# Performance work log

Hardware: AMD Instinct MI355X
Metric: run time of the kernel (lower is better)

## Reference

```python
import jax, jax.numpy as jnp
import numpy as np

N_NODES = 10000
N_EDGES = 80000
IN_DIM = 1024
HID = 4096
OUT = 256


def sage_conv(x, src, dst, W_l, b_l, W_r, num_nodes):
    # mean aggregation of source-node features onto target nodes
    msg = x[src]                                            # [E, D] gather
    agg = jax.ops.segment_sum(msg, dst, num_segments=num_nodes)   # [N, D]
    cnt = jax.ops.segment_sum(jnp.ones((src.shape[0],), x.dtype), dst,
                              num_segments=num_nodes)       # [N]
    mean = agg / jnp.clip(cnt, 1.0)[:, None]                # isolated nodes -> 0
    # lin_l(mean) + lin_r(x); lin_r has no bias in PyG SAGEConv
    return mean @ W_l.T + b_l + x @ W_r.T


def setup_inputs() -> dict:
    key = jax.random.key(0)
    ks = jax.random.split(key, 6)
    x = jax.random.normal(ks[0], (N_NODES, IN_DIM), dtype=jnp.float32)
    edge_index = jax.random.randint(ks[1], (2, N_EDGES), 0, N_NODES, dtype=jnp.int32)
    s1 = 1.0 / np.sqrt(IN_DIM)
    s2 = 1.0 / np.sqrt(HID)
    W1_l = jax.random.normal(ks[2], (HID, IN_DIM), dtype=jnp.float32) * s1
    b1_l = jnp.zeros((HID,), jnp.float32)
    W1_r = jax.random.normal(ks[3], (HID, IN_DIM), dtype=jnp.float32) * s1
    W2_l = jax.random.normal(ks[4], (OUT, HID), dtype=jnp.float32) * s2
    b2_l = jnp.zeros((OUT,), jnp.float32)
    W2_r = jax.random.normal(ks[5], (OUT, HID), dtype=jnp.float32) * s2
    return {"x": x, "edge_index": edge_index, "W1_l": W1_l, "b1_l": b1_l,
            "W1_r": W1_r, "W2_l": W2_l, "b2_l": b2_l, "W2_r": W2_r}


def reference(x, edge_index, W1_l, b1_l, W1_r, W2_l, b2_l, W2_r):
    src, dst = edge_index[0], edge_index[1]
    h = sage_conv(x, src, dst, W1_l, b1_l, W1_r, N_NODES)   # [N, 4096]
    h = jax.nn.relu(h)
    # dropout is identity in eval mode
    out = sage_conv(h, src, dst, W2_l, b2_l, W2_r, N_NODES)  # [N, 256]
    return jax.nn.log_softmax(out, axis=1)
```

## Files before the change

### kernel.cpp

```cpp
#include <hip/hip_runtime.h>
#include <cstdint>
#include <cstddef>

#define DEVINL __device__ __forceinline__

typedef __bf16 bf16x8 __attribute__((ext_vector_type(8)));
typedef float f32x4 __attribute__((ext_vector_type(4)));

static constexpr int NN = 10000;
static constexpr int NE = 80000;
static constexpr int IN_DIM = 1024;
static constexpr int HID = 4096;
static constexpr int OUTD = 256;
static constexpr int M_PAD = 10112;

DEVINL unsigned short f2bf(float f) {
  unsigned int u = __builtin_bit_cast(unsigned int, f);
  u += 0x7fffu + ((u >> 16) & 1u);
  return (unsigned short)(u >> 16);
}
DEVINL float bf2f(unsigned short h) {
  unsigned int u = ((unsigned int)h) << 16;
  return __builtin_bit_cast(float, u);
}

DEVINL void ld_lds16(const void* g, void* l) {
  __builtin_amdgcn_global_load_lds(
      (const __attribute__((address_space(1))) unsigned int*)g,
      (__attribute__((address_space(3))) unsigned int*)l, 16, 0, 0);
}

static constexpr int PREP_B1 = 8192;
static constexpr int PREP_B2 = PREP_B1 + 2048;
static constexpr int PREP_B3 = PREP_B2 + 10000;
static constexpr int PREP_NB = PREP_B3 + 313;

__global__ __launch_bounds__(256) void prep_kernel(
    const float* __restrict__ W1l, const float* __restrict__ W1r,
    const float* __restrict__ W2l, const float* __restrict__ W2r,
    const float* __restrict__ x, const int* __restrict__ dst,
    unsigned short* __restrict__ w1cat, unsigned short* __restrict__ w2cat,
    unsigned short* __restrict__ x_bf, int* __restrict__ deg) {
  int b = blockIdx.x;
  int t = threadIdx.x;
  if (b < PREP_B1) {
    int g = b * 256 + t;
    int n = g >> 9;
    int kg = g & 511;
    const float* s = (kg < 256) ? (W1l + (size_t)n * 1024 + kg * 4)
                                : (W1r + (size_t)n * 1024 + (kg - 256) * 4);
    float4 v = *(const float4*)s;
    ushort4 p = {f2bf(v.x), f2bf(v.y), f2bf(v.z), f2bf(v.w)};
    ((ushort4*)w1cat)[g] = p;
  } else if (b < PREP_B2) {
    int g = (b - PREP_B1) * 256 + t;
    int n = g >> 10;
    int kg = g & 1023;
    const float* s = (n < 256) ? (W2l + (size_t)n * 4096 + kg * 4)
                               : (W2r + (size_t)(n - 256) * 4096 + kg * 4);
    float4 v = *(const float4*)s;
    ushort4 p = {f2bf(v.x), f2bf(v.y), f2bf(v.z), f2bf(v.w)};
    ((ushort4*)w2cat)[g] = p;
  } else if (b < PREP_B3) {
    int g = (b - PREP_B2) * 256 + t;
    int i = g >> 8;
    int kg = g & 255;
    float4 v = ((const float4*)(x + (size_t)i * IN_DIM))[kg];
    ushort4 p = {f2bf(v.x), f2bf(v.y), f2bf(v.z), f2bf(v.w)};
    ((ushort4*)(x_bf + (size_t)i * IN_DIM))[kg] = p;
  } else {
    int e = (b - PREP_B3) * 256 + t;
    if (e < NE) atomicAdd(&deg[dst[e]], 1);
  }
}

__global__ __launch_bounds__(1024) void scan_kernel(const int* __restrict__ deg,
                                                    int* __restrict__ offs,
                                                    int* __restrict__ cur) {
  __shared__ int part[1024];
  constexpr int NPT = 10;
  int t = threadIdx.x;
  int base = t * NPT;
  int s = 0;
  for (int j = 0; j < NPT; ++j) {
    int n = base + j;
    s += (n < NN) ? deg[n] : 0;
  }
  part[t] = s;
  __syncthreads();
  for (int o = 1; o < 1024; o <<= 1) {
    int v = (t >= o) ? part[t - o] : 0;
    __syncthreads();
    part[t] += v;
    __syncthreads();
  }
  int pre = (t > 0) ? part[t - 1] : 0;
  for (int j = 0; j < NPT; ++j) {
    int n = base + j;
    if (n < NN) {
      offs[n] = pre;
      cur[n] = pre;
      pre += deg[n];
    }
  }
  if (t == 1023) offs[NN] = part[1023];
}

__global__ void bin_kernel(const int* __restrict__ src, const int* __restrict__ dst,
                           int* __restrict__ cur, int* __restrict__ csr) {
  int e = blockIdx.x * 256 + threadIdx.x;
  if (e < NE) {
    int p = atomicAdd(&cur[dst[e]], 1);
    csr[p] = src[e];
  }
}

__global__ __launch_bounds__(256) void gather1_kernel(unsigned short* __restrict__ x_bf,
                                                      const int* __restrict__ offs,
                                                      const int* __restrict__ csr,
                                                      unsigned short* __restrict__ A1) {
  int i = blockIdx.x;
  int t = threadIdx.x;
  unsigned short* row = A1 + (size_t)i * 1024;
  if (i >= NN) {
    ushort4 z = {0, 0, 0, 0};
    ((ushort4*)row)[t] = z;
    ((ushort4*)(x_bf + (size_t)i * 1024))[t] = z;
    return;
  }
  int beg = offs[i], end = offs[i + 1];
  float4 a0 = {0.f, 0.f, 0.f, 0.f}, a1 = {0.f, 0.f, 0.f, 0.f};
  int j = beg;
  for (; j + 2 <= end; j += 2) {
    int s0 = __builtin_amdgcn_readfirstlane(csr[j]);
    int s1 = __builtin_amdgcn_readfirstlane(csr[j + 1]);
    ushort4 u0 = ((const ushort4*)(x_bf + (size_t)s0 * IN_DIM))[t];
    ushort4 u1 = ((const ushort4*)(x_bf + (size_t)s1 * IN_DIM))[t];
    a0.x += bf2f(u0.x); a0.y += bf2f(u0.y); a0.z += bf2f(u0.z); a0.w += bf2f(u0.w);
    a1.x += bf2f(u1.x); a1.y += bf2f(u1.y); a1.z += bf2f(u1.z); a1.w += bf2f(u1.w);
  }
  if (j < end) {
    int s0 = __builtin_amdgcn_readfirstlane(csr[j]);
    ushort4 u0 = ((const ushort4*)(x_bf + (size_t)s0 * IN_DIM))[t];
    a0.x += bf2f(u0.x); a0.y += bf2f(u0.y); a0.z += bf2f(u0.z); a0.w += bf2f(u0.w);
  }
  float inv = 1.0f / (float)max(end - beg, 1);
  ushort4 pa = {f2bf((a0.x + a1.x) * inv), f2bf((a0.y + a1.y) * inv),
                f2bf((a0.z + a1.z) * inv), f2bf((a0.w + a1.w) * inv)};
  ((ushort4*)row)[t] = pa;
}

__global__ __launch_bounds__(256) void gemm1_pipe_kernel(
    const unsigned short* __restrict__ A,
    const unsigned short* __restrict__ A2,
    const unsigned short* __restrict__ Bt,
    const float* __restrict__ bias,
    unsigned short* __restrict__ C) {
  constexpr int BM = 128, BN = 128, BK = 64;
  constexpr int K = 2048, N = 4096;
  constexpr int NT = K / BK;
  constexpr int NUMM = 79, NUMN = 32, GM = 32, NPG = GM * NUMN;
  constexpr int TSZ = BM * BK;

  __shared__ unsigned short Asm[2 * TSZ];
  __shared__ unsigned short Bsm[3 * TSZ];

  const int pid = blockIdx.x;
  const int gid = pid / NPG;
  const int first_m = gid * GM;
  const int sz = (NUMM - first_m < GM) ? (NUMM - first_m) : GM;
  const int local = pid % NPG;
  const int pm = first_m + local % sz;
  const int pn = local / sz;
  const long tm0 = (long)pm * BM;
  const long tn0 = (long)pn * BN;

  const int tid = threadIdx.x;
  const int lane = tid & 63;
  const int wave = tid >> 6;
  const int quad = lane >> 4;
  const int l16 = lane & 15;
  const int l7 = l16 & 7;
  const int wm = (wave % 2) * 64;
  const int wn = (wave / 2) * 64;

  f32x4 acc[4][4];
#pragma unroll
  for (int i = 0; i < 4; ++i)
#pragma unroll
    for (int j = 0; j < 4; ++j) acc[i][j] = (f32x4){0.f, 0.f, 0.f, 0.f};

  size_t aOff[4], bOff[4];
#pragma unroll
  for (int s = 0; s < 4; ++s) {
    int c = s * 256 + tid;
    int r = c >> 3;
    int g = (c & 7) ^ (r & 7);
    aOff[s] = (size_t)(tm0 + r) * 1024 + g * 8;
    bOff[s] = (size_t)(tn0 + r) * K + g * 8;
  }

#define STAGE_A1(kt, ab)                                                            \
  {                                                                                 \
    const unsigned short* s_ = ((kt) < NT / 2) ? A : A2;                            \
    const int ka_ = ((kt) & (NT / 2 - 1)) * BK;                                     \
    _Pragma("unroll") for (int q_ = 0; q_ < 4; ++q_)                                \
        ld_lds16(s_ + aOff[q_] + ka_, Asm + (ab)*TSZ + q_ * 2048 + wave * 512);     \
  }
#define STAGE_B1(kt, bb)                                                            \
  {                                                                                 \
    const int k0_ = (kt)*BK;                                                        \
    _Pragma("unroll") for (int q_ = 0; q_ < 4; ++q_)                                \
        ld_lds16(Bt + bOff[q_] + k0_, Bsm + (bb)*TSZ + q_ * 2048 + wave * 512);     \
  }

  STAGE_A1(0, 0)
  STAGE_B1(0, 0)
  STAGE_B1(1, 1)

  int bb = 0;
  for (int t = 0; t < NT; ++t) {
    if (t + 1 < NT) STAGE_A1(t + 1, (t + 1) & 1)
    if (t + 2 < NT) {
      int bb2 = bb + 2;
      if (bb2 >= 3) bb2 -= 3;
      STAGE_B1(t + 2, bb2)
    }
    if (t + 2 < NT) {
      asm volatile("s_waitcnt vmcnt(12)" ::: "memory");
    } else if (t + 1 < NT) {
      asm volatile("s_waitcnt vmcnt(8)" ::: "memory");
    } else {
      asm volatile("s_waitcnt vmcnt(0)" ::: "memory");
    }
    __builtin_amdgcn_s_barrier();
    __builtin_amdgcn_sched_barrier(0);

    const unsigned short* As = Asm + (t & 1) * TSZ;
    const unsigned short* Bs = Bsm + bb * TSZ;
#pragma unroll
    for (int kk = 0; kk < 2; ++kk) {
      const int p = (kk * 4 + quad) ^ l7;
      bf16x8 af[4], bv[4];
#pragma unroll
      for (int i = 0; i < 4; ++i) af[i] = *(const bf16x8*)(As + (wm + i * 16 + l16) * BK + p * 8);
#pragma unroll
      for (int j = 0; j < 4; ++j) bv[j] = *(const bf16x8*)(Bs + (wn + j * 16 + l16) * BK + p * 8);
#pragma unroll
      for (int i = 0; i < 4; ++i)
#pragma unroll
        for (int j = 0; j < 4; ++j)
          acc[i][j] = __builtin_amdgcn_mfma_f32_16x16x32_bf16(af[i], bv[j], acc[i][j], 0, 0, 0);
    }
    __builtin_amdgcn_s_barrier();
    __builtin_amdgcn_sched_barrier(0);
    bb = (bb == 2) ? 0 : bb + 1;
  }
#undef STAGE_A1
#undef STAGE_B1

#pragma unroll
  for (int i = 0; i < 4; ++i) {
    long m0 = tm0 + wm + i * 16 + quad * 4;
#pragma unroll
    for (int j = 0; j < 4; ++j) {
      int n = (int)tn0 + wn + j * 16 + l16;
      float bvs = bias[n];
#pragma unroll
      for (int r = 0; r < 4; ++r) {
        float v = fmaxf(acc[i][j][r] + bvs, 0.0f);
        C[(size_t)(m0 + r) * N + n] = f2bf(v);
      }
    }
  }
}

template <int BM, int BN, int BK, int K, int KSPLIT, int N, int NUMM, int NUMN, int GM,
          int EPI, int NWY, bool ASPLIT>
__global__ __launch_bounds__(256) void gemm_kernel(const unsigned short* __restrict__ A,
                                                   const unsigned short* __restrict__ A2,
                                                   const unsigned short* __restrict__ Bt,
                                                   const float* __restrict__ bias,
                                                   void* __restrict__ C0out) {
  constexpr int MGR = 4 / NWY;
  constexpr int MI = BM / 16 / MGR;
  constexpr int NI = 4;
  constexpr int CPR = BK / 8;
  constexpr int SA = BM * CPR / 256;
  constexpr int SB = BN * CPR / 256;
  constexpr int KK = BK / 32;
  constexpr int KS = K / KSPLIT;
  constexpr int AS = ASPLIT ? K / 2 : K;
  __shared__ unsigned short Asm[BM * BK];
  __shared__ unsigned short Bsm[BN * BK];

  constexpr int NPG = GM * NUMN;
  const int pid = blockIdx.x;
  const int gid = pid / NPG;
  const int first_m = gid * GM;
  const int sz = (NUMM - first_m < GM) ? (NUMM - first_m) : GM;
  const int local = pid % NPG;
  const int pm = first_m + local % sz;
  const int pn = local / sz;
  const int koff = (KSPLIT > 1) ? (int)blockIdx.y * KS : 0;

  const int tid = threadIdx.x;
  const int lane = tid & 63;
  const int wave = tid >> 6;
  const int quad = lane >> 4;
  const int l16 = lane & 15;
  const int wm = (wave % MGR) * (BM / MGR);
  const int wn = (wave / MGR) * 64;
  const long tm0 = (long)pm * BM;
  const long tn0 = (long)pn * BN;

  f32x4 acc[MI][NI];
#pragma unroll
  for (int i = 0; i < MI; ++i)
#pragma unroll
    for (int j = 0; j < NI; ++j) acc[i][j] = (f32x4){0.f, 0.f, 0.f, 0.f};

  size_t aOff[SA];
  unsigned short* aDst[SA];
  const unsigned short* bSrc[SB];
  unsigned short* bDst[SB];
#pragma unroll
  for (int s = 0; s < SA; ++s) {
    int c = s * 256 + wave * 64 + lane;
    int r = c / CPR;
    int g = (c % CPR) ^ (r & 7);
    aOff[s] = (size_t)(tm0 + r) * AS + koff + g * 8;
    aDst[s] = Asm + s * 2048 + wave * 512;
  }
#pragma unroll
  for (int s = 0; s < SB; ++s) {
    int c = s * 256 + wave * 64 + lane;
    int r = c / CPR;
    int g = (c % CPR) ^ (r & 7);
    bSrc[s] = Bt + (size_t)(tn0 + r) * K + koff + g * 8;
    bDst[s] = Bsm + s * 2048 + wave * 512;
  }

  const int l7 = l16 & 7;

  for (int k0 = 0; k0 < KS; k0 += BK) {
    const unsigned short* ab = (!ASPLIT || k0 < K / 2) ? A : A2;
    const int ka = ASPLIT ? (k0 & (K / 2 - 1)) : k0;
#pragma unroll
    for (int s = 0; s < SA; ++s) ld_lds16(ab + aOff[s] + ka, aDst[s]);
#pragma unroll
    for (int s = 0; s < SB; ++s) ld_lds16(bSrc[s] + k0, bDst[s]);
    __syncthreads();

#pragma unroll
    for (int kk = 0; kk < KK; ++kk) {
      const int p = (kk * 4 + quad) ^ l7;
      bf16x8 af[MI], bv[NI];
#pragma unroll
      for (int i = 0; i < MI; ++i) {
        int ra = wm + i * 16 + l16;
        af[i] = *(const bf16x8*)(Asm + ra * BK + p * 8);
      }
#pragma unroll
      for (int j = 0; j < NI; ++j) {
        int rb = wn + j * 16 + l16;
        bv[j] = *(const bf16x8*)(Bsm + rb * BK + p * 8);
      }
#pragma unroll
      for (int i = 0; i < MI; ++i)
#pragma unroll
        for (int j = 0; j < NI; ++j)
          acc[i][j] = __builtin_amdgcn_mfma_f32_16x16x32_bf16(af[i], bv[j], acc[i][j], 0, 0, 0);
    }
    __syncthreads();
  }

  if (EPI == 1) {
    unsigned short* C = (unsigned short*)C0out;
#pragma unroll
    for (int i = 0; i < MI; ++i) {
      long m0 = tm0 + wm + i * 16 + quad * 4;
#pragma unroll
      for (int j = 0; j < NI; ++j) {
        int n = (int)tn0 + wn + j * 16 + l16;
        float bvs = bias[n];
#pragma unroll
        for (int r = 0; r < 4; ++r) {
          float v = acc[i][j][r] + bvs;
          v = fmaxf(v, 0.0f);
          C[(size_t)(m0 + r) * N + n] = f2bf(v);
        }
      }
    }
  } else {
    unsigned short* C = (unsigned short*)C0out + (size_t)blockIdx.y * NUMM * BM * N;
#pragma unroll
    for (int i = 0; i < MI; ++i) {
      long m0 = tm0 + wm + i * 16 + quad * 4;
#pragma unroll
      for (int j = 0; j < NI; ++j) {
        int n = (int)tn0 + wn + j * 16 + l16;
#pragma unroll
        for (int r = 0; r < 4; ++r) C[(size_t)(m0 + r) * N + n] = f2bf(acc[i][j][r]);
      }
    }
  }
}

__global__ __launch_bounds__(128) void gather2_final_kernel(const unsigned short* __restrict__ P,
                                                            const int* __restrict__ offs,
                                                            const int* __restrict__ csr,
                                                            const float* __restrict__ b2,
                                                            float* __restrict__ out) {
  int i = blockIdx.x;
  int t = threadIdx.x;
  const unsigned short* P1 = P + (size_t)M_PAD * 512;
  int beg = offs[i], end = offs[i + 1];
  float a0 = 0.f, a1 = 0.f, c0 = 0.f, c1 = 0.f;
  int j = beg;
  for (; j + 2 <= end; j += 2) {
    int s0 = __builtin_amdgcn_readfirstlane(csr[j]);
    int s1 = __builtin_amdgcn_readfirstlane(csr[j + 1]);
    unsigned int u0 = ((const unsigned int*)(P + (size_t)s0 * 512))[t];
    unsigned int w0 = ((const unsigned int*)(P1 + (size_t)s0 * 512))[t];
    unsigned int u1 = ((const unsigned int*)(P + (size_t)s1 * 512))[t];
    unsigned int w1 = ((const unsigned int*)(P1 + (size_t)s1 * 512))[t];
    a0 += bf2f((unsigned short)(u0 & 0xffffu)) + bf2f((unsigned short)(w0 & 0xffffu));
    a1 += bf2f((unsigned short)(u0 >> 16)) + bf2f((unsigned short)(w0 >> 16));
    c0 += bf2f((unsigned short)(u1 & 0xffffu)) + bf2f((unsigned short)(w1 & 0xffffu));
    c1 += bf2f((unsigned short)(u1 >> 16)) + bf2f((unsigned short)(w1 >> 16));
  }
  if (j < end) {
    int s0 = __builtin_amdgcn_readfirstlane(csr[j]);
    unsigned int u0 = ((const unsigned int*)(P + (size_t)s0 * 512))[t];
    unsigned int w0 = ((const unsigned int*)(P1 + (size_t)s0 * 512))[t];
    a0 += bf2f((unsigned short)(u0 & 0xffffu)) + bf2f((unsigned short)(w0 & 0xffffu));
    a1 += bf2f((unsigned short)(u0 >> 16)) + bf2f((unsigned short)(w0 >> 16));
  }
  float inv = 1.0f / (float)max(end - beg, 1);
  float2 bv = ((const float2*)b2)[t];
  unsigned int su = ((const unsigned int*)(P + (size_t)i * 512))[128 + t];
  unsigned int sw = ((const unsigned int*)(P1 + (size_t)i * 512))[128 + t];
  float pv0 = bf2f((unsigned short)(su & 0xffffu)) + bf2f((unsigned short)(sw & 0xffffu));
  float pv1 = bf2f((unsigned short)(su >> 16)) + bf2f((unsigned short)(sw >> 16));
  float v0 = (a0 + c0) * inv + bv.x + pv0;
  float v1 = (a1 + c1) * inv + bv.y + pv1;

  __shared__ float sm[2], ss[2];
  int w = t >> 6;
  float m = fmaxf(v0, v1);
#pragma unroll
  for (int o = 32; o > 0; o >>= 1) m = fmaxf(m, __shfl_xor(m, o, 64));
  if ((t & 63) == 0) sm[w] = m;
  __syncthreads();
  m = fmaxf(sm[0], sm[1]);

  float s = __expf(v0 - m) + __expf(v1 - m);
#pragma unroll
  for (int o = 32; o > 0; o >>= 1) s += __shfl_xor(s, o, 64);
  if ((t & 63) == 0) ss[w] = s;
  __syncthreads();
  float ls = logf(ss[0] + ss[1]);

  float2 o2 = {v0 - m - ls, v1 - m - ls};
  ((float2*)(out + (size_t)i * OUTD))[t] = o2;
}

static constexpr size_t OFF_A1 = 0;
static constexpr size_t OFF_XBF = OFF_A1 + (size_t)M_PAD * 1024 * 2;
static constexpr size_t OFF_W1 = OFF_XBF + (size_t)M_PAD * 1024 * 2;
static constexpr size_t OFF_HB = OFF_W1 + (size_t)HID * 2048 * 2;
static constexpr size_t OFF_W2 = OFF_HB + (size_t)M_PAD * HID * 2;
static constexpr size_t OFF_DEG = OFF_W2 + (size_t)512 * HID * 2;
static constexpr size_t OFF_OFFS = OFF_DEG + (size_t)NN * 4;
static constexpr size_t OFF_CUR = OFF_OFFS + (size_t)(NN + 4) * 4;
static constexpr size_t OFF_CSR = OFF_CUR + (size_t)NN * 4;
static constexpr size_t OFF_P = OFF_A1;

extern "C" void kernel_launch(void* const* d_in, const int* in_sizes, int n_in,
                              void* d_out, int out_size, void* d_ws, size_t ws_size,
                              hipStream_t stream) {
  const float* x = (const float*)d_in[0];
  const int* ei = (const int*)d_in[1];
  const int* src = ei;
  const int* dst = ei + NE;
  const float* W1_l = (const float*)d_in[2];
  const float* b1_l = (const float*)d_in[3];
  const float* W1_r = (const float*)d_in[4];
  const float* W2_l = (const float*)d_in[5];
  const float* b2_l = (const float*)d_in[6];
  const float* W2_r = (const float*)d_in[7];
  float* out = (float*)d_out;

  char* ws = (char*)d_ws;
  unsigned short* A1 = (unsigned short*)(ws + OFF_A1);
  unsigned short* x_bf = (unsigned short*)(ws + OFF_XBF);
  unsigned short* w1cat = (unsigned short*)(ws + OFF_W1);
  unsigned short* h_b = (unsigned short*)(ws + OFF_HB);
  unsigned short* w2cat = (unsigned short*)(ws + OFF_W2);
  int* deg = (int*)(ws + OFF_DEG);
  int* offs = (int*)(ws + OFF_OFFS);
  int* cur = (int*)(ws + OFF_CUR);
  int* csr = (int*)(ws + OFF_CSR);
  unsigned short* P = (unsigned short*)(ws + OFF_P);

  hipMemsetAsync(deg, 0, (size_t)NN * 4, stream);

  prep_kernel<<<PREP_NB, 256, 0, stream>>>(W1_l, W1_r, W2_l, W2_r, x, dst,
                                           w1cat, w2cat, x_bf, deg);
  scan_kernel<<<1, 1024, 0, stream>>>(deg, offs, cur);
  bin_kernel<<<(NE + 255) / 256, 256, 0, stream>>>(src, dst, cur, csr);

  gather1_kernel<<<M_PAD, 256, 0, stream>>>(x_bf, offs, csr, A1);

  gemm1_pipe_kernel<<<79 * 32, 256, 0, stream>>>(A1, x_bf, w1cat, b1_l, h_b);

  gemm_kernel<64, 256, 64, 4096, 2, 512, 158, 2, 1, 3, 4, false>
      <<<dim3(158 * 2, 2), 256, 0, stream>>>(h_b, nullptr, w2cat, nullptr, P);

  gather2_final_kernel<<<NN, 128, 0, stream>>>(P, offs, csr, b2_l, out);
}
```

Before: 444.8 us.

## Load GEMM1 A fragments directly into registers, double-buffer only B in LDS

The first GEMM now reads its A operand straight from global memory into registers each k-step, instead of staging it through shared memory. The B operand pipeline drops from triple to double buffering. This cuts LDS usage and LDS traffic, which may allow more resident blocks. In exchange, A loads are not prefetched a step ahead, so their global latency sits on the critical path. Waves that share the same rows also fetch those A rows redundantly.

```diff
diff --git a/kernel.cpp b/kernel.cpp
--- a/kernel.cpp
+++ b/kernel.cpp
@@ -150,7 +150,7 @@
   ((ushort4*)row)[t] = pa;
 }
 
-__global__ __launch_bounds__(256) void gemm1_pipe_kernel(
+__global__ __launch_bounds__(256) void gemm1_areg_kernel(
     const unsigned short* __restrict__ A,
     const unsigned short* __restrict__ A2,
     const unsigned short* __restrict__ Bt,
@@ -160,10 +160,9 @@
   constexpr int K = 2048, N = 4096;
   constexpr int NT = K / BK;
   constexpr int NUMM = 79, NUMN = 32, GM = 32, NPG = GM * NUMN;
-  constexpr int TSZ = BM * BK;
-
-  __shared__ unsigned short Asm[2 * TSZ];
-  __shared__ unsigned short Bsm[3 * TSZ];
+  constexpr int TSZ = BN * BK;
+
+  __shared__ unsigned short Bsm[2 * TSZ];
 
   const int pid = blockIdx.x;
   const int gid = pid / NPG;
@@ -190,73 +189,66 @@
 #pragma unroll
     for (int j = 0; j < 4; ++j) acc[i][j] = (f32x4){0.f, 0.f, 0.f, 0.f};
 
-  size_t aOff[4], bOff[4];
+  size_t bOff[4];
 #pragma unroll
   for (int s = 0; s < 4; ++s) {
     int c = s * 256 + tid;
     int r = c >> 3;
     int g = (c & 7) ^ (r & 7);
-    aOff[s] = (size_t)(tm0 + r) * 1024 + g * 8;
     bOff[s] = (size_t)(tn0 + r) * K + g * 8;
   }
 
-#define STAGE_A1(kt, ab)                                                            \
-  {                                                                                 \
-    const unsigned short* s_ = ((kt) < NT / 2) ? A : A2;                            \
-    const int ka_ = ((kt) & (NT / 2 - 1)) * BK;                                     \
-    _Pragma("unroll") for (int q_ = 0; q_ < 4; ++q_)                                \
-        ld_lds16(s_ + aOff[q_] + ka_, Asm + (ab)*TSZ + q_ * 2048 + wave * 512);     \
-  }
-#define STAGE_B1(kt, bb)                                                            \
-  {                                                                                 \
-    const int k0_ = (kt)*BK;                                                        \
-    _Pragma("unroll") for (int q_ = 0; q_ < 4; ++q_)                                \
-        ld_lds16(Bt + bOff[q_] + k0_, Bsm + (bb)*TSZ + q_ * 2048 + wave * 512);     \
-  }
-
-  STAGE_A1(0, 0)
+  size_t aRow[4];
+#pragma unroll
+  for (int i = 0; i < 4; ++i)
+    aRow[i] = (size_t)(tm0 + wm + i * 16 + l16) * 1024 + quad * 8;
+
+#define STAGE_B1(kt, bb)                                                         \
+  {                                                                              \
+    const int k0_ = (kt)*BK;                                                     \
+    _Pragma("unroll") for (int q_ = 0; q_ < 4; ++q_)                             \
+        ld_lds16(Bt + bOff[q_] + k0_, Bsm + (bb)*TSZ + q_ * 2048 + wave * 512);  \
+  }
+
   STAGE_B1(0, 0)
-  STAGE_B1(1, 1)
-
-  int bb = 0;
+
   for (int t = 0; t < NT; ++t) {
-    if (t + 1 < NT) STAGE_A1(t + 1, (t + 1) & 1)
-    if (t + 2 < NT) {
-      int bb2 = bb + 2;
-      if (bb2 >= 3) bb2 -= 3;
-      STAGE_B1(t + 2, bb2)
-    }
-    if (t + 2 < NT) {
+    const unsigned short* As = (t < NT / 2) ? A : A2;
+    const int ka = (t & (NT / 2 - 1)) * BK;
+    bf16x8 af[2][4];
+#pragma unroll
+    for (int kk = 0; kk < 2; ++kk)
+#pragma unroll
+      for (int i = 0; i < 4; ++i)
+        af[kk][i] = *(const bf16x8*)(As + aRow[i] + ka + kk * 32);
+    __builtin_amdgcn_sched_barrier(0);
+
+    if (t + 1 < NT) {
+      STAGE_B1(t + 1, (t + 1) & 1)
       asm volatile("s_waitcnt vmcnt(12)" ::: "memory");
-    } else if (t + 1 < NT) {
+    } else {
       asm volatile("s_waitcnt vmcnt(8)" ::: "memory");
-    } else {
-      asm volatile("s_waitcnt vmcnt(0)" ::: "memory");
     }
     __builtin_amdgcn_s_barrier();
     __builtin_amdgcn_sched_barrier(0);
 
-    const unsigned short* As = Asm + (t & 1) * TSZ;
-    const unsigned short* Bs = Bsm + bb * TSZ;
+    const unsigned short* Bs = Bsm + (t & 1) * TSZ;
 #pragma unroll
     for (int kk = 0; kk < 2; ++kk) {
       const int p = (kk * 4 + quad) ^ l7;
-      bf16x8 af[4], bv[4];
-#pragma unroll
-      for (int i = 0; i < 4; ++i) af[i] = *(const bf16x8*)(As + (wm + i * 16 + l16) * BK + p * 8);
-#pragma unroll
-      for (int j = 0; j < 4; ++j) bv[j] = *(const bf16x8*)(Bs + (wn + j * 16 + l16) * BK + p * 8);
+      bf16x8 bv[4];
+#pragma unroll
+      for (int j = 0; j < 4; ++j)
+        bv[j] = *(const bf16x8*)(Bs + (wn + j * 16 + l16) * BK + p * 8);
 #pragma unroll
       for (int i = 0; i < 4; ++i)
 #pragma unroll
         for (int j = 0; j < 4; ++j)
-          acc[i][j] = __builtin_amdgcn_mfma_f32_16x16x32_bf16(af[i], bv[j], acc[i][j], 0, 0, 0);
+          acc[i][j] = __builtin_amdgcn_mfma_f32_16x16x32_bf16(af[kk][i], bv[j], acc[i][j], 0, 0, 0);
     }
     __builtin_amdgcn_s_barrier();
     __builtin_amdgcn_sched_barrier(0);
-    bb = (bb == 2) ? 0 : bb + 1;
-  }
-#undef STAGE_A1
+  }
 #undef STAGE_B1
 
 #pragma unroll
@@ -513,7 +505,7 @@
 
   gather1_kernel<<<M_PAD, 256, 0, stream>>>(x_bf, offs, csr, A1);
 
-  gemm1_pipe_kernel<<<79 * 32, 256, 0, stream>>>(A1, x_bf, w1cat, b1_l, h_b);
+  gemm1_areg_kernel<<<79 * 32, 256, 0, stream>>>(A1, x_bf, w1cat, b1_l, h_b);
 
   gemm_kernel<64, 256, 64, 4096, 2, 512, 158, 2, 1, 3, 4, false>
       <<<dim3(158 * 2, 2), 256, 0, stream>>>(h_b, nullptr, w2cat, nullptr, P);
```

Result: slower. 598.8 us (+34.6%).

## Double-buffer second GEMM loads and shrink final gather to one wave

Applied to the files above, without the earlier changes.

Replaces the generic templated GEMM for the second layer with a specialized kernel that double-buffers A/B tiles in LDS, issuing the next tile's global-to-LDS loads before computing on the current one and waiting with a partial vmcnt. This aims to overlap memory latency with MFMA work, at the cost of doubled LDS usage (80KB), which may reduce occupancy. The final gather/log-softmax kernel now uses a single 64-thread wave with 4 elements per lane, which removes the LDS cross-wave reductions and barriers.

```diff
diff --git a/kernel.cpp b/kernel.cpp
--- a/kernel.cpp
+++ b/kernel.cpp
@@ -23,6 +23,8 @@
   unsigned int u = ((unsigned int)h) << 16;
   return __builtin_bit_cast(float, u);
 }
+DEVINL float bflo(unsigned int u) { return bf2f((unsigned short)(u & 0xffffu)); }
+DEVINL float bfhi(unsigned int u) { return bf2f((unsigned short)(u >> 16)); }
 
 DEVINL void ld_lds16(const void* g, void* l) {
   __builtin_amdgcn_global_load_lds(
@@ -275,195 +277,162 @@
   }
 }
 
-template <int BM, int BN, int BK, int K, int KSPLIT, int N, int NUMM, int NUMN, int GM,
-          int EPI, int NWY, bool ASPLIT>
-__global__ __launch_bounds__(256) void gemm_kernel(const unsigned short* __restrict__ A,
-                                                   const unsigned short* __restrict__ A2,
-                                                   const unsigned short* __restrict__ Bt,
-                                                   const float* __restrict__ bias,
-                                                   void* __restrict__ C0out) {
-  constexpr int MGR = 4 / NWY;
-  constexpr int MI = BM / 16 / MGR;
-  constexpr int NI = 4;
-  constexpr int CPR = BK / 8;
-  constexpr int SA = BM * CPR / 256;
-  constexpr int SB = BN * CPR / 256;
-  constexpr int KK = BK / 32;
-  constexpr int KS = K / KSPLIT;
-  constexpr int AS = ASPLIT ? K / 2 : K;
-  __shared__ unsigned short Asm[BM * BK];
-  __shared__ unsigned short Bsm[BN * BK];
-
-  constexpr int NPG = GM * NUMN;
+__global__ __launch_bounds__(256) void gemm2_pipe_kernel(
+    const unsigned short* __restrict__ A,
+    const unsigned short* __restrict__ Bt,
+    unsigned short* __restrict__ P) {
+  constexpr int BM = 64, BN = 256, BK = 64;
+  constexpr int K = 4096, N = 512;
+  constexpr int KS = 2048;
+  constexpr int NT = KS / BK;
+  constexpr int ATS = BM * BK;
+  constexpr int BTS = BN * BK;
+  __shared__ unsigned short Asm[2 * ATS];
+  __shared__ unsigned short Bsm[2 * BTS];
+
   const int pid = blockIdx.x;
-  const int gid = pid / NPG;
-  const int first_m = gid * GM;
-  const int sz = (NUMM - first_m < GM) ? (NUMM - first_m) : GM;
-  const int local = pid % NPG;
-  const int pm = first_m + local % sz;
-  const int pn = local / sz;
-  const int koff = (KSPLIT > 1) ? (int)blockIdx.y * KS : 0;
+  const int pm = pid >> 1;
+  const int pn = pid & 1;
+  const int koff = (int)blockIdx.y * KS;
+  const long tm0 = (long)pm * BM;
+  const long tn0 = (long)pn * BN;
 
   const int tid = threadIdx.x;
   const int lane = tid & 63;
   const int wave = tid >> 6;
   const int quad = lane >> 4;
   const int l16 = lane & 15;
-  const int wm = (wave % MGR) * (BM / MGR);
-  const int wn = (wave / MGR) * 64;
-  const long tm0 = (long)pm * BM;
-  const long tn0 = (long)pn * BN;
-
-  f32x4 acc[MI][NI];
-#pragma unroll
-  for (int i = 0; i < MI; ++i)
-#pragma unroll
-    for (int j = 0; j < NI; ++j) acc[i][j] = (f32x4){0.f, 0.f, 0.f, 0.f};
-
-  size_t aOff[SA];
-  unsigned short* aDst[SA];
-  const unsigned short* bSrc[SB];
-  unsigned short* bDst[SB];
-#pragma unroll
-  for (int s = 0; s < SA; ++s) {
-    int c = s * 256 + wave * 64 + lane;
-    int r = c / CPR;
-    int g = (c % CPR) ^ (r & 7);
-    aOff[s] = (size_t)(tm0 + r) * AS + koff + g * 8;
-    aDst[s] = Asm + s * 2048 + wave * 512;
-  }
-#pragma unroll
-  for (int s = 0; s < SB; ++s) {
-    int c = s * 256 + wave * 64 + lane;
-    int r = c / CPR;
-    int g = (c % CPR) ^ (r & 7);
-    bSrc[s] = Bt + (size_t)(tn0 + r) * K + koff + g * 8;
-    bDst[s] = Bsm + s * 2048 + wave * 512;
-  }
-
   const int l7 = l16 & 7;
-
-  for (int k0 = 0; k0 < KS; k0 += BK) {
-    const unsigned short* ab = (!ASPLIT || k0 < K / 2) ? A : A2;
-    const int ka = ASPLIT ? (k0 & (K / 2 - 1)) : k0;
-#pragma unroll
-    for (int s = 0; s < SA; ++s) ld_lds16(ab + aOff[s] + ka, aDst[s]);
-#pragma unroll
-    for (int s = 0; s < SB; ++s) ld_lds16(bSrc[s] + k0, bDst[s]);
-    __syncthreads();
-
-#pragma unroll
-    for (int kk = 0; kk < KK; ++kk) {
+  const int wn = wave * 64;
+
+  f32x4 acc[4][4];
+#pragma unroll
+  for (int i = 0; i < 4; ++i)
+#pragma unroll
+    for (int j = 0; j < 4; ++j) acc[i][j] = (f32x4){0.f, 0.f, 0.f, 0.f};
+
+  size_t aOff[2], bOff[8];
+#pragma unroll
+  for (int s = 0; s < 2; ++s) {
+    int c = s * 256 + tid;
+    int r = c >> 3;
+    int g = (c & 7) ^ (r & 7);
+    aOff[s] = (size_t)(tm0 + r) * K + koff + g * 8;
+  }
+#pragma unroll
+  for (int s = 0; s < 8; ++s) {
+    int c = s * 256 + tid;
+    int r = c >> 3;
+    int g = (c & 7) ^ (r & 7);
+    bOff[s] = (size_t)(tn0 + r) * K + koff + g * 8;
+  }
+
+#define STAGE2(kt, buf)                                                              \
+  {                                                                                  \
+    const int k0_ = (kt)*BK;                                                         \
+    _Pragma("unroll") for (int s_ = 0; s_ < 2; ++s_)                                 \
+        ld_lds16(A + aOff[s_] + k0_, Asm + (buf)*ATS + s_ * 2048 + wave * 512);      \
+    _Pragma("unroll") for (int s_ = 0; s_ < 8; ++s_)                                 \
+        ld_lds16(Bt + bOff[s_] + k0_, Bsm + (buf)*BTS + s_ * 2048 + wave * 512);     \
+  }
+
+  STAGE2(0, 0)
+
+  for (int t = 0; t < NT; ++t) {
+    if (t + 1 < NT) {
+      STAGE2(t + 1, (t + 1) & 1)
+      asm volatile("s_waitcnt vmcnt(10)" ::: "memory");
+    } else {
+      asm volatile("s_waitcnt vmcnt(0)" ::: "memory");
+    }
+    __builtin_amdgcn_s_barrier();
+    __builtin_amdgcn_sched_barrier(0);
+
+    const unsigned short* As = Asm + (t & 1) * ATS;
+    const unsigned short* Bs = Bsm + (t & 1) * BTS;
+#pragma unroll
+    for (int kk = 0; kk < 2; ++kk) {
       const int p = (kk * 4 + quad) ^ l7;
-      bf16x8 af[MI], bv[NI];
-#pragma unroll
-      for (int i = 0; i < MI; ++i) {
-        int ra = wm + i * 16 + l16;
-        af[i] = *(const bf16x8*)(Asm + ra * BK + p * 8);
-      }
-#pragma unroll
-      for (int j = 0; j < NI; ++j) {
-        int rb = wn + j * 16 + l16;
-        bv[j] = *(const bf16x8*)(Bsm + rb * BK + p * 8);
-      }
-#pragma unroll
-      for (int i = 0; i < MI; ++i)
-#pragma unroll
-        for (int j = 0; j < NI; ++j)
+      bf16x8 af[4], bv[4];
+#pragma unroll
+      for (int i = 0; i < 4; ++i) af[i] = *(const bf16x8*)(As + (i * 16 + l16) * BK + p * 8);
+#pragma unroll
+      for (int j = 0; j < 4; ++j) bv[j] = *(const bf16x8*)(Bs + (wn + j * 16 + l16) * BK + p * 8);
+#pragma unroll
+      for (int i = 0; i < 4; ++i)
+#pragma unroll
+        for (int j = 0; j < 4; ++j)
           acc[i][j] = __builtin_amdgcn_mfma_f32_16x16x32_bf16(af[i], bv[j], acc[i][j], 0, 0, 0);
     }
-    __syncthreads();
-  }
-
-  if (EPI == 1) {
-    unsigned short* C = (unsigned short*)C0out;
-#pragma unroll
-    for (int i = 0; i < MI; ++i) {
-      long m0 = tm0 + wm + i * 16 + quad * 4;
-#pragma unroll
-      for (int j = 0; j < NI; ++j) {
-        int n = (int)tn0 + wn + j * 16 + l16;
-        float bvs = bias[n];
-#pragma unroll
-        for (int r = 0; r < 4; ++r) {
-          float v = acc[i][j][r] + bvs;
-          v = fmaxf(v, 0.0f);
-          C[(size_t)(m0 + r) * N + n] = f2bf(v);
-        }
-      }
-    }
-  } else {
-    unsigned short* C = (unsigned short*)C0out + (size_t)blockIdx.y * NUMM * BM * N;
-#pragma unroll
-    for (int i = 0; i < MI; ++i) {
-      long m0 = tm0 + wm + i * 16 + quad * 4;
-#pragma unroll
-      for (int j = 0; j < NI; ++j) {
-        int n = (int)tn0 + wn + j * 16 + l16;
-#pragma unroll
-        for (int r = 0; r < 4; ++r) C[(size_t)(m0 + r) * N + n] = f2bf(acc[i][j][r]);
-      }
-    }
-  }
-}
-
-__global__ __launch_bounds__(128) void gather2_final_kernel(const unsigned short* __restrict__ P,
-                                                            const int* __restrict__ offs,
-                                                            const int* __restrict__ csr,
-                                                            const float* __restrict__ b2,
-                                                            float* __restrict__ out) {
+    __builtin_amdgcn_s_barrier();
+    __builtin_amdgcn_sched_barrier(0);
+  }
+#undef STAGE2
+
+  unsigned short* C = P + (size_t)blockIdx.y * M_PAD * 512;
+#pragma unroll
+  for (int i = 0; i < 4; ++i) {
+    long m0 = tm0 + i * 16 + quad * 4;
+#pragma unroll
+    for (int j = 0; j < 4; ++j) {
+      int n = (int)tn0 + wn + j * 16 + l16;
+#pragma unroll
+      for (int r = 0; r < 4; ++r) C[(size_t)(m0 + r) * N + n] = f2bf(acc[i][j][r]);
+    }
+  }
+}
+
+__global__ __launch_bounds__(64) void gather2_final_kernel(const unsigned short* __restrict__ P,
+                                                           const int* __restrict__ offs,
+                                                           const int* __restrict__ csr,
+                                                           const float* __restrict__ b2,
+                                                           float* __restrict__ out) {
   int i = blockIdx.x;
   int t = threadIdx.x;
   const unsigned short* P1 = P + (size_t)M_PAD * 512;
   int beg = offs[i], end = offs[i + 1];
-  float a0 = 0.f, a1 = 0.f, c0 = 0.f, c1 = 0.f;
+  float a0 = 0.f, a1 = 0.f, a2 = 0.f, a3 = 0.f;
   int j = beg;
   for (; j + 2 <= end; j += 2) {
     int s0 = __builtin_amdgcn_readfirstlane(csr[j]);
     int s1 = __builtin_amdgcn_readfirstlane(csr[j + 1]);
-    unsigned int u0 = ((const unsigned int*)(P + (size_t)s0 * 512))[t];
-    unsigned int w0 = ((const unsigned int*)(P1 + (size_t)s0 * 512))[t];
-    unsigned int u1 = ((const unsigned int*)(P + (size_t)s1 * 512))[t];
-    unsigned int w1 = ((const unsigned int*)(P1 + (size_t)s1 * 512))[t];
-    a0 += bf2f((unsigned short)(u0 & 0xffffu)) + bf2f((unsigned short)(w0 & 0xffffu));
-    a1 += bf2f((unsigned short)(u0 >> 16)) + bf2f((unsigned short)(w0 >> 16));
-    c0 += bf2f((unsigned short)(u1 & 0xffffu)) + bf2f((unsigned short)(w1 & 0xffffu));
-    c1 += bf2f((unsigned short)(u1 >> 16)) + bf2f((unsigned short)(w1 >> 16));
+    uint2 u0 = *(const uint2*)(P + (size_t)s0 * 512 + 4 * t);
+    uint2 w0 = *(const uint2*)(P1 + (size_t)s0 * 512 + 4 * t);
+    uint2 u1 = *(const uint2*)(P + (size_t)s1 * 512 + 4 * t);
+    uint2 w1 = *(const uint2*)(P1 + (size_t)s1 * 512 + 4 * t);
+    a0 += bflo(u0.x) + bflo(w0.x) + bflo(u1.x) + bflo(w1.x);
+    a1 += bfhi(u0.x) + bfhi(w0.x) + bfhi(u1.x) + bfhi(w1.x);
+    a2 += bflo(u0.y) + bflo(w0.y) + bflo(u1.y) + bflo(w1.y);
+    a3 += bfhi(u0.y) + bfhi(w0.y) + bfhi(u1.y) + bfhi(w1.y);
   }
   if (j < end) {
     int s0 = __builtin_amdgcn_readfirstlane(csr[j]);
-    unsigned int u0 = ((const unsigned int*)(P + (size_t)s0 * 512))[t];
-    unsigned int w0 = ((const unsigned int*)(P1 + (size_t)s0 * 512))[t];
-    a0 += bf2f((unsigned short)(u0 & 0xffffu)) + bf2f((unsigned short)(w0 & 0xffffu));
-    a1 += bf2f((unsigned short)(u0 >> 16)) + bf2f((unsigned short)(w0 >> 16));
+    uint2 u0 = *(const uint2*)(P + (size_t)s0 * 512 + 4 * t);
+    uint2 w0 = *(const uint2*)(P1 + (size_t)s0 * 512 + 4 * t);
+    a0 += bflo(u0.x) + bflo(w0.x);
+    a1 += bfhi(u0.x) + bfhi(w0.x);
+    a2 += bflo(u0.y) + bflo(w0.y);
+    a3 += bfhi(u0.y) + bfhi(w0.y);
   }
   float inv = 1.0f / (float)max(end - beg, 1);
-  float2 bv = ((const float2*)b2)[t];
-  unsigned int su = ((const unsigned int*)(P + (size_t)i * 512))[128 + t];
-  unsigned int sw = ((const unsigned int*)(P1 + (size_t)i * 512))[128 + t];
-  float pv0 = bf2f((unsigned short)(su & 0xffffu)) + bf2f((unsigned short)(sw & 0xffffu));
-  float pv1 = bf2f((unsigned short)(su >> 16)) + bf2f((unsigned short)(sw >> 16));
-  float v0 = (a0 + c0) * inv + bv.x + pv0;
-  float v1 = (a1 + c1) * inv + bv.y + pv1;
-
-  __shared__ float sm[2], ss[2];
-  int w = t >> 6;
-  float m = fmaxf(v0, v1);
+  float4 bv = ((const float4*)b2)[t];
+  uint2 su = *(const uint2*)(P + (size_t)i * 512 + 256 + 4 * t);
+  uint2 sw = *(const uint2*)(P1 + (size_t)i * 512 + 256 + 4 * t);
+  float v0 = a0 * inv + bv.x + bflo(su.x) + bflo(sw.x);
+  float v1 = a1 * inv + bv.y + bfhi(su.x) + bfhi(sw.x);
+  float v2 = a2 * inv + bv.z + bflo(su.y) + bflo(sw.y);
+  float v3 = a3 * inv + bv.w + bfhi(su.y) + bfhi(sw.y);
+
+  float m = fmaxf(fmaxf(v0, v1), fmaxf(v2, v3));
 #pragma unroll
   for (int o = 32; o > 0; o >>= 1) m = fmaxf(m, __shfl_xor(m, o, 64));
-  if ((t & 63) == 0) sm[w] = m;
-  __syncthreads();
-  m = fmaxf(sm[0], sm[1]);
-
-  float s = __expf(v0 - m) + __expf(v1 - m);
+  float s = __expf(v0 - m) + __expf(v1 - m) + __expf(v2 - m) + __expf(v3 - m);
 #pragma unroll
   for (int o = 32; o > 0; o >>= 1) s += __shfl_xor(s, o, 64);
-  if ((t & 63) == 0) ss[w] = s;
-  __syncthreads();
-  float ls = logf(ss[0] + ss[1]);
-
-  float2 o2 = {v0 - m - ls, v1 - m - ls};
-  ((float2*)(out + (size_t)i * OUTD))[t] = o2;
+  float ls = logf(s);
+
+  float4 o4 = {v0 - m - ls, v1 - m - ls, v2 - m - ls, v3 - m - ls};
+  ((float4*)(out + (size_t)i * OUTD))[t] = o4;
 }
 
 static constexpr size_t OFF_A1 = 0;
@@ -515,8 +484,7 @@
 
   gemm1_pipe_kernel<<<79 * 32, 256, 0, stream>>>(A1, x_bf, w1cat, b1_l, h_b);
 
-  gemm_kernel<64, 256, 64, 4096, 2, 512, 158, 2, 1, 3, 4, false>
-      <<<dim3(158 * 2, 2), 256, 0, stream>>>(h_b, nullptr, w2cat, nullptr, P);
-
-  gather2_final_kernel<<<NN, 128, 0, stream>>>(P, offs, csr, b2_l, out);
-}
+  gemm2_pipe_kernel<<<dim3(158 * 2, 2), 256, 0, stream>>>(h_b, w2cat, P);
+
+  gather2_final_kernel<<<NN, 64, 0, stream>>>(P, offs, csr, b2_l, out);
+}
```

Result: slower. 458.0 us (+3.0%).
